# Kernel optimization log

Hardware: AMD Instinct MI355X
Metric: run time of the kernel (lower is better)

## Reference

```python
import jax, jax.numpy as jnp
import numpy as np

EMBED_DIM = 1024
HEAD_DIM = 64
B, T = 4, 4096


def setup_inputs() -> dict:
    key = jax.random.key(0)
    kx, kq, kk, kv = jax.random.split(key, 4)
    x = jax.random.normal(kx, (B, T, EMBED_DIM), dtype=jnp.float32)
    # nn.Linear weights, stored transposed as (in, out) for x @ W
    s = 1.0 / np.sqrt(EMBED_DIM)
    Wq = jax.random.normal(kq, (EMBED_DIM, HEAD_DIM), dtype=jnp.float32) * s
    Wk = jax.random.normal(kk, (EMBED_DIM, HEAD_DIM), dtype=jnp.float32) * s
    Wv = jax.random.normal(kv, (EMBED_DIM, HEAD_DIM), dtype=jnp.float32) * s
    return {"x": x, "Wq": Wq, "Wk": Wk, "Wv": Wv}


def reference(x, Wq, Wk, Wv):
    Bc, Tc, C = x.shape
    Q = x @ Wq  # [B, T, H]
    K = x @ Wk
    V = x @ Wv
    # NOTE: original scales by embedding_dim C, not head_dim
    scores = jnp.einsum('bqh,bkh->bqk', Q, K) / jnp.sqrt(jnp.float32(C))
    causal = jnp.tril(jnp.ones((Tc, Tc), dtype=bool))
    scores = jnp.where(causal, scores, -jnp.inf)
    attn = jax.nn.softmax(scores, axis=-1)
    return jnp.einsum('bqk,bkh->bqh', attn, V)
```

## Files before the change

kernel.cpp:

```cpp
#include <hip/hip_runtime.h>
#include <hip/hip_bf16.h>
#include <math.h>

typedef __attribute__((ext_vector_type(8))) short bf16x8;
typedef __attribute__((ext_vector_type(4))) float f32x4;

#define MFMA16 __builtin_amdgcn_mfma_f32_16x16x32_bf16

static constexpr int TSEQ = 4096;
static constexpr int EMB = 1024;
static constexpr int HD = 64;

__device__ __forceinline__ unsigned short f2bf(float f) {
    unsigned u = __builtin_bit_cast(unsigned, f);
    u += 0x7fffu + ((u >> 16) & 1u);
    return (unsigned short)(u >> 16);
}
__device__ __forceinline__ int pk2bf(float a, float b) {
    return (int)((unsigned)f2bf(a) | ((unsigned)f2bf(b) << 16));
}

union frag_u { int i[4]; bf16x8 v; };

__global__ void prep_w(const float* __restrict__ Wq, const float* __restrict__ Wk,
                       const float* __restrict__ Wv, unsigned short* __restrict__ Wp) {
    int id = blockIdx.x * 256 + threadIdx.x;
    int wsel = id >> 16;
    int t = id & 65535;
    int k = t >> 6, n0 = t & 63;
    const float* W = (wsel == 0) ? Wq : (wsel == 1) ? Wk : Wv;
    float v = W[t];
    if (wsel == 0) v *= 0.03125f;
    int n = wsel * 64 + n0;
    Wp[(k >> 5) * 6144 + n * 32 + (k & 31)] = f2bf(v);
}

__global__ __launch_bounds__(256, 2) void proj_kernel(const float* __restrict__ X,
        const unsigned short* __restrict__ Wp, unsigned short* __restrict__ Qp,
        unsigned short* __restrict__ Kp, unsigned short* __restrict__ Vp) {
    const int lane = threadIdx.x & 63, wave = threadIdx.x >> 6;
    const int col = lane & 15, quad = lane >> 4;
    const int row0 = blockIdx.x * 32;

    f32x4 acc[2][3];
#pragma unroll
    for (int m = 0; m < 2; m++)
#pragma unroll
        for (int j = 0; j < 3; j++) acc[m][j] = (f32x4)(0.0f);

    const float* xr0 = X + (size_t)(row0 + col) * EMB + quad * 8;
    const float* xr1 = xr0 + 16 * EMB;
    const char* wB = (const char*)Wp + wave * 1024 + col * 64 + quad * 16;

    float4 xa[2][2];
    bf16x8 wf[3];
    xa[0][0] = *(const float4*)(xr0);
    xa[0][1] = *(const float4*)(xr0 + 4);
    xa[1][0] = *(const float4*)(xr1);
    xa[1][1] = *(const float4*)(xr1 + 4);
#pragma unroll
    for (int j = 0; j < 3; j++) wf[j] = *(const bf16x8*)(wB + j * 4096);

#pragma unroll 2
    for (int kc = 0; kc < 32; kc++) {
        float4 xn[2][2];
        bf16x8 wn[3];
        if (kc < 31) {
            const float* p0 = xr0 + (kc + 1) * 32;
            const float* p1 = xr1 + (kc + 1) * 32;
            xn[0][0] = *(const float4*)(p0);
            xn[0][1] = *(const float4*)(p0 + 4);
            xn[1][0] = *(const float4*)(p1);
            xn[1][1] = *(const float4*)(p1 + 4);
            const char* wp = wB + (size_t)(kc + 1) * 12288;
#pragma unroll
            for (int j = 0; j < 3; j++) wn[j] = *(const bf16x8*)(wp + j * 4096);
        }
        frag_u A[2];
#pragma unroll
        for (int m = 0; m < 2; m++) {
            A[m].i[0] = pk2bf(xa[m][0].x, xa[m][0].y);
            A[m].i[1] = pk2bf(xa[m][0].z, xa[m][0].w);
            A[m].i[2] = pk2bf(xa[m][1].x, xa[m][1].y);
            A[m].i[3] = pk2bf(xa[m][1].z, xa[m][1].w);
        }
#pragma unroll
        for (int m = 0; m < 2; m++)
#pragma unroll
            for (int j = 0; j < 3; j++)
                acc[m][j] = MFMA16(A[m].v, wf[j], acc[m][j], 0, 0, 0);
        if (kc < 31) {
#pragma unroll
            for (int m = 0; m < 2; m++)
#pragma unroll
                for (int h = 0; h < 2; h++) xa[m][h] = xn[m][h];
#pragma unroll
            for (int j = 0; j < 3; j++) wf[j] = wn[j];
        }
    }

    const int tile0 = blockIdx.x * 2;
    const int c = blockIdx.x;
#pragma unroll
    for (int m = 0; m < 2; m++) {
#pragma unroll
        for (int r = 0; r < 4; r++)
            Qp[(tile0 + m) * 1024 + (wave >> 1) * 512 + (quad * 4 + r) * 32 +
               ((wave & 1) * 2 + (col >> 3)) * 8 + (col & 7)] = f2bf(acc[m][0][r]);
#pragma unroll
        for (int r = 0; r < 4; r++)
            Kp[((c * 2 + m) * 2 + (wave >> 1)) * 512 + (quad * 4 + r) * 32 +
               ((wave & 1) * 2 + (col >> 3)) * 8 + (col & 7)] = f2bf(acc[m][1][r]);
        ushort4 pk;
        pk.x = f2bf(acc[m][2][0]); pk.y = f2bf(acc[m][2][1]);
        pk.z = f2bf(acc[m][2][2]); pk.w = f2bf(acc[m][2][3]);
        *(ushort4*)&Vp[c * 2048 + wave * 512 + col * 32 + m * 16 + quad * 4] = pk;
    }
}

__global__ __launch_bounds__(512, 4) void attn_kernel(const unsigned short* __restrict__ Qp,
        const unsigned short* __restrict__ Kp, const unsigned short* __restrict__ Vp,
        float* __restrict__ Out) {
    __shared__ float cmb[4][2][64][20];
    __shared__ unsigned short plds[8][2][640];
    const int lane = threadIdx.x & 63, wave = threadIdx.x >> 6;
    const int col = lane & 15, quad = lane >> 4;
    const int batch = blockIdx.x & 3;
    const int ti = 127 - (blockIdx.x >> 2);
    const int q0 = ti * 32;
    const size_t bT = (size_t)batch * TSEQ;
    const int fragoff = col * 64 + quad * 16;

    const char* QpB = (const char*)Qp;
    const char* KpB = (const char*)Kp;
    const char* VpB = (const char*)Vp;
    const int gt = (int)((bT + q0) >> 4);
    const int c0 = (int)(bT >> 5);

    bf16x8 aq[2][2];
#pragma unroll
    for (int m = 0; m < 2; m++)
#pragma unroll
        for (int h = 0; h < 2; h++)
            aq[m][h] = *(const bf16x8*)(QpB + (size_t)((gt + m) * 2 + h) * 1024 + fragoff);

    f32x4 o[2][4];
    f32x4 lsum[2];
#pragma unroll
    for (int m = 0; m < 2; m++) {
        lsum[m] = (f32x4)(0.0f);
#pragma unroll
        for (int t = 0; t < 4; t++) o[m][t] = (f32x4)(0.0f);
    }

    for (int c = wave; c <= ti; c += 8) {
        const char* kb = KpB + (size_t)(c0 + c) * 4096;
        const char* vb = VpB + (size_t)(c0 + c) * 4096;
        bf16x8 bk[2][2], bv[4];
#pragma unroll
        for (int j = 0; j < 2; j++)
#pragma unroll
            for (int h = 0; h < 2; h++)
                bk[j][h] = *(const bf16x8*)(kb + j * 2048 + h * 1024 + fragoff);
#pragma unroll
        for (int t = 0; t < 4; t++)
            bv[t] = *(const bf16x8*)(vb + t * 1024 + fragoff);

        f32x4 s[2][2];
#pragma unroll
        for (int m = 0; m < 2; m++)
#pragma unroll
            for (int j = 0; j < 2; j++) {
                f32x4 a = MFMA16(aq[m][0], bk[j][0], (f32x4)(0.0f), 0, 0, 0);
                s[m][j] = MFMA16(aq[m][1], bk[j][1], a, 0, 0, 0);
            }
        const bool diag = (c == ti);
#pragma unroll
        for (int m = 0; m < 2; m++)
#pragma unroll
            for (int j = 0; j < 2; j++)
#pragma unroll
                for (int r = 0; r < 4; r++) {
                    float v = s[m][j][r];
                    if (diag && (j * 16 + col > m * 16 + quad * 4 + r)) v = -INFINITY;
                    const float p = __expf(v);
                    lsum[m][r] += p;
                    plds[wave][m][(quad * 4 + r) * 40 + j * 16 + col] =
                        (unsigned short)(__builtin_bit_cast(unsigned, p) >> 16);
                }
        bf16x8 pa[2];
#pragma unroll
        for (int m = 0; m < 2; m++)
            pa[m] = *(const bf16x8*)(&plds[wave][m][col * 40 + quad * 8]);
#pragma unroll
        for (int m = 0; m < 2; m++)
#pragma unroll
            for (int t = 0; t < 4; t++)
                o[m][t] = MFMA16(pa[m], bv[t], o[m][t], 0, 0, 0);
    }

    auto wr = [&](int s) {
#pragma unroll
        for (int m = 0; m < 2; m++) {
#pragma unroll
            for (int t = 0; t < 4; t++)
                *(f32x4*)&cmb[s][m][lane][t * 4] = o[m][t];
            *(f32x4*)&cmb[s][m][lane][16] = lsum[m];
        }
    };
    auto rd = [&](int s) {
#pragma unroll
        for (int m = 0; m < 2; m++) {
#pragma unroll
            for (int t = 0; t < 4; t++)
                o[m][t] += *(const f32x4*)&cmb[s][m][lane][t * 4];
            lsum[m] += *(const f32x4*)&cmb[s][m][lane][16];
        }
    };
    if (wave >= 4) wr(wave - 4);
    __syncthreads();
    if (wave < 4) rd(wave);
    __syncthreads();
    if (wave == 2 || wave == 3) wr(wave);
    __syncthreads();
    if (wave < 2) rd(wave + 2);
    __syncthreads();
    if (wave == 1) wr(1);
    __syncthreads();
    if (wave == 0) {
        rd(1);
#pragma unroll
        for (int off = 1; off < 16; off <<= 1)
#pragma unroll
            for (int m = 0; m < 2; m++)
#pragma unroll
                for (int r = 0; r < 4; r++)
                    lsum[m][r] += __shfl_xor(lsum[m][r], off, 64);
#pragma unroll
        for (int m = 0; m < 2; m++)
#pragma unroll
            for (int r = 0; r < 4; r++) {
                const float inv = 1.0f / lsum[m][r];
                const size_t orow = (bT + q0 + m * 16 + quad * 4 + r) * HD;
#pragma unroll
                for (int t = 0; t < 4; t++)
                    Out[orow + t * 16 + col] = o[m][t][r] * inv;
            }
    }
}

extern "C" void kernel_launch(void* const* d_in, const int* in_sizes, int n_in,
                              void* d_out, int out_size, void* d_ws, size_t ws_size,
                              hipStream_t stream) {
    const float* x  = (const float*)d_in[0];
    const float* Wq = (const float*)d_in[1];
    const float* Wk = (const float*)d_in[2];
    const float* Wv = (const float*)d_in[3];
    float* out = (float*)d_out;

    char* w = (char*)d_ws;
    unsigned short* Wp = (unsigned short*)(w);
    unsigned short* Qp = (unsigned short*)(w + (512 << 10));
    unsigned short* Kp = (unsigned short*)(w + (512 << 10) + (2 << 20));
    unsigned short* Vp = (unsigned short*)(w + (512 << 10) + (4 << 20));

    hipLaunchKernelGGL(prep_w, dim3(768), dim3(256), 0, stream, Wq, Wk, Wv, Wp);
    hipLaunchKernelGGL(proj_kernel, dim3(512), dim3(256), 0, stream, x, Wp, Qp, Kp, Vp);
    hipLaunchKernelGGL(attn_kernel, dim3(512), dim3(512), 0, stream, Qp, Kp, Vp, out);
}
```

Measured before the change: 162.7 us.

## Stage projection weights in LDS via async global_load_lds with split-K waves

The projection kernel now doubles its block to 512 threads and splits the K dimension between two wave groups. Each stage of packed weights is copied straight into double-buffered shared memory with global_load_lds, and the two partial accumulators are summed through LDS before the store. prep_w writes the weights in a fragment-friendly layout so each lane reads one contiguous 16-byte fragment. The goal is to cut redundant global weight loads and add memory parallelism, at the cost of two barriers per stage and an extra LDS reduction.

```diff
diff --git a/kernel.cpp b/kernel.cpp
--- a/kernel.cpp
+++ b/kernel.cpp
@@ -21,6 +21,12 @@
 }
 
 union frag_u { int i[4]; bf16x8 v; };
+
+__device__ __forceinline__ void gll16(const void* g, void* l) {
+    __builtin_amdgcn_global_load_lds(
+        (const __attribute__((address_space(1))) void*)g,
+        (__attribute__((address_space(3))) void*)l, 16, 0, 0);
+}
 
 __global__ void prep_w(const float* __restrict__ Wq, const float* __restrict__ Wk,
                        const float* __restrict__ Wv, unsigned short* __restrict__ Wp) {
@@ -32,14 +38,18 @@
     float v = W[t];
     if (wsel == 0) v *= 0.03125f;
     int n = wsel * 64 + n0;
-    Wp[(k >> 5) * 6144 + n * 32 + (k & 31)] = f2bf(v);
-}
-
-__global__ __launch_bounds__(256, 2) void proj_kernel(const float* __restrict__ X,
+    Wp[(k >> 5) * 6144 + (n >> 4) * 512 + ((k >> 3) & 3) * 128 + (n & 15) * 8 + (k & 7)] = f2bf(v);
+}
+
+__global__ __launch_bounds__(512, 4) void proj_kernel(const float* __restrict__ X,
         const unsigned short* __restrict__ Wp, unsigned short* __restrict__ Qp,
         unsigned short* __restrict__ Kp, unsigned short* __restrict__ Vp) {
-    const int lane = threadIdx.x & 63, wave = threadIdx.x >> 6;
+    __shared__ unsigned short wlds[2][12288];
+
+    const int tid = threadIdx.x;
+    const int lane = tid & 63, wave = tid >> 6;
     const int col = lane & 15, quad = lane >> 4;
+    const int par = wave >> 2, ng = wave & 3;
     const int row0 = blockIdx.x * 32;
 
     f32x4 acc[2][3];
@@ -48,73 +58,97 @@
 #pragma unroll
         for (int j = 0; j < 3; j++) acc[m][j] = (f32x4)(0.0f);
 
-    const float* xr0 = X + (size_t)(row0 + col) * EMB + quad * 8;
-    const float* xr1 = xr0 + 16 * EMB;
-    const char* wB = (const char*)Wp + wave * 1024 + col * 64 + quad * 16;
-
-    float4 xa[2][2];
-    bf16x8 wf[3];
-    xa[0][0] = *(const float4*)(xr0);
-    xa[0][1] = *(const float4*)(xr0 + 4);
-    xa[1][0] = *(const float4*)(xr1);
-    xa[1][1] = *(const float4*)(xr1 + 4);
-#pragma unroll
-    for (int j = 0; j < 3; j++) wf[j] = *(const bf16x8*)(wB + j * 4096);
-
-#pragma unroll 2
-    for (int kc = 0; kc < 32; kc++) {
-        float4 xn[2][2];
-        bf16x8 wn[3];
-        if (kc < 31) {
-            const float* p0 = xr0 + (kc + 1) * 32;
-            const float* p1 = xr1 + (kc + 1) * 32;
-            xn[0][0] = *(const float4*)(p0);
-            xn[0][1] = *(const float4*)(p0 + 4);
-            xn[1][0] = *(const float4*)(p1);
-            xn[1][1] = *(const float4*)(p1 + 4);
-            const char* wp = wB + (size_t)(kc + 1) * 12288;
-#pragma unroll
-            for (int j = 0; j < 3; j++) wn[j] = *(const bf16x8*)(wp + j * 4096);
-        }
-        frag_u A[2];
+    const char* wsrc = (const char*)Wp + lane * 16;
+    auto stageW = [&](int s, int b) {
+        const char* src = wsrc + (size_t)(2 * s + par) * 12288;
+        char* d = (char*)&wlds[b][0] + par * 12288;
+        gll16(src + ng * 1024,       d + ng * 1024);
+        gll16(src + (4 + ng) * 1024, d + (4 + ng) * 1024);
+        gll16(src + (8 + ng) * 1024, d + (8 + ng) * 1024);
+    };
+
+    const float* xs0 = X + (size_t)(row0 + col) * EMB + par * 32 + quad * 8;
+    const float* xs1 = xs0 + 16 * EMB;
+
+    auto compute = [&](int b, float4 a00, float4 a01, float4 a10, float4 a11) {
+        frag_u A0, A1;
+        A0.i[0] = pk2bf(a00.x, a00.y); A0.i[1] = pk2bf(a00.z, a00.w);
+        A0.i[2] = pk2bf(a01.x, a01.y); A0.i[3] = pk2bf(a01.z, a01.w);
+        A1.i[0] = pk2bf(a10.x, a10.y); A1.i[1] = pk2bf(a10.z, a10.w);
+        A1.i[2] = pk2bf(a11.x, a11.y); A1.i[3] = pk2bf(a11.z, a11.w);
+        const char* wb = (const char*)&wlds[b][0] + par * 12288 + lane * 16;
+        const bf16x8 W0 = *(const bf16x8*)(wb + ng * 1024);
+        const bf16x8 W1 = *(const bf16x8*)(wb + (4 + ng) * 1024);
+        const bf16x8 W2 = *(const bf16x8*)(wb + (8 + ng) * 1024);
+        acc[0][0] = MFMA16(A0.v, W0, acc[0][0], 0, 0, 0);
+        acc[0][1] = MFMA16(A0.v, W1, acc[0][1], 0, 0, 0);
+        acc[0][2] = MFMA16(A0.v, W2, acc[0][2], 0, 0, 0);
+        acc[1][0] = MFMA16(A1.v, W0, acc[1][0], 0, 0, 0);
+        acc[1][1] = MFMA16(A1.v, W1, acc[1][1], 0, 0, 0);
+        acc[1][2] = MFMA16(A1.v, W2, acc[1][2], 0, 0, 0);
+    };
+
+    float4 p00, p01, p10, p11, q00, q01, q10, q11;
+    stageW(0, 0);
+    p00 = *(const float4*)(xs0);
+    p01 = *(const float4*)(xs0 + 4);
+    p10 = *(const float4*)(xs1);
+    p11 = *(const float4*)(xs1 + 4);
+    __syncthreads();
+
+    for (int si = 0; si < 8; si++) {
+        const int s0 = si * 2;
+        if (s0 + 1 < 16) {
+            q00 = *(const float4*)(xs0 + (s0 + 1) * 64);
+            q01 = *(const float4*)(xs0 + (s0 + 1) * 64 + 4);
+            q10 = *(const float4*)(xs1 + (s0 + 1) * 64);
+            q11 = *(const float4*)(xs1 + (s0 + 1) * 64 + 4);
+            stageW(s0 + 1, 1);
+        }
+        compute(0, p00, p01, p10, p11);
+        __syncthreads();
+        if (s0 + 2 < 16) {
+            p00 = *(const float4*)(xs0 + (s0 + 2) * 64);
+            p01 = *(const float4*)(xs0 + (s0 + 2) * 64 + 4);
+            p10 = *(const float4*)(xs1 + (s0 + 2) * 64);
+            p11 = *(const float4*)(xs1 + (s0 + 2) * 64 + 4);
+            stageW(s0 + 2, 0);
+        }
+        compute(1, q00, q01, q10, q11);
+        __syncthreads();
+    }
+
+    f32x4* ex = (f32x4*)&wlds[0][0];
+    if (par == 1) {
+#pragma unroll
+        for (int m = 0; m < 2; m++)
+#pragma unroll
+            for (int j = 0; j < 3; j++)
+                ex[(m * 3 + j) * 256 + ng * 64 + lane] = acc[m][j];
+    }
+    __syncthreads();
+    if (par == 0) {
+#pragma unroll
+        for (int m = 0; m < 2; m++)
+#pragma unroll
+            for (int j = 0; j < 3; j++)
+                acc[m][j] += ex[(m * 3 + j) * 256 + ng * 64 + lane];
 #pragma unroll
         for (int m = 0; m < 2; m++) {
-            A[m].i[0] = pk2bf(xa[m][0].x, xa[m][0].y);
-            A[m].i[1] = pk2bf(xa[m][0].z, xa[m][0].w);
-            A[m].i[2] = pk2bf(xa[m][1].x, xa[m][1].y);
-            A[m].i[3] = pk2bf(xa[m][1].z, xa[m][1].w);
-        }
-#pragma unroll
-        for (int m = 0; m < 2; m++)
-#pragma unroll
-            for (int j = 0; j < 3; j++)
-                acc[m][j] = MFMA16(A[m].v, wf[j], acc[m][j], 0, 0, 0);
-        if (kc < 31) {
-#pragma unroll
-            for (int m = 0; m < 2; m++)
-#pragma unroll
-                for (int h = 0; h < 2; h++) xa[m][h] = xn[m][h];
-#pragma unroll
-            for (int j = 0; j < 3; j++) wf[j] = wn[j];
-        }
-    }
-
-    const int tile0 = blockIdx.x * 2;
-    const int c = blockIdx.x;
-#pragma unroll
-    for (int m = 0; m < 2; m++) {
-#pragma unroll
-        for (int r = 0; r < 4; r++)
-            Qp[(tile0 + m) * 1024 + (wave >> 1) * 512 + (quad * 4 + r) * 32 +
-               ((wave & 1) * 2 + (col >> 3)) * 8 + (col & 7)] = f2bf(acc[m][0][r]);
-#pragma unroll
-        for (int r = 0; r < 4; r++)
-            Kp[((c * 2 + m) * 2 + (wave >> 1)) * 512 + (quad * 4 + r) * 32 +
-               ((wave & 1) * 2 + (col >> 3)) * 8 + (col & 7)] = f2bf(acc[m][1][r]);
-        ushort4 pk;
-        pk.x = f2bf(acc[m][2][0]); pk.y = f2bf(acc[m][2][1]);
-        pk.z = f2bf(acc[m][2][2]); pk.w = f2bf(acc[m][2][3]);
-        *(ushort4*)&Vp[c * 2048 + wave * 512 + col * 32 + m * 16 + quad * 4] = pk;
+            const int tile = blockIdx.x * 2 + m;
+#pragma unroll
+            for (int r = 0; r < 4; r++)
+                Qp[tile * 1024 + (ng >> 1) * 512 + (quad * 4 + r) * 32 +
+                   ((ng & 1) * 2 + (col >> 3)) * 8 + (col & 7)] = f2bf(acc[m][0][r]);
+#pragma unroll
+            for (int r = 0; r < 4; r++)
+                Kp[(tile * 2 + (ng >> 1)) * 512 + (quad * 4 + r) * 32 +
+                   ((ng & 1) * 2 + (col >> 3)) * 8 + (col & 7)] = f2bf(acc[m][1][r]);
+            ushort4 pk;
+            pk.x = f2bf(acc[m][2][0]); pk.y = f2bf(acc[m][2][1]);
+            pk.z = f2bf(acc[m][2][2]); pk.w = f2bf(acc[m][2][3]);
+            *(ushort4*)&Vp[blockIdx.x * 2048 + ng * 512 + col * 32 + m * 16 + quad * 4] = pk;
+        }
     }
 }
 
@@ -265,6 +299,6 @@
     unsigned short* Vp = (unsigned short*)(w + (512 << 10) + (4 << 20));
 
     hipLaunchKernelGGL(prep_w, dim3(768), dim3(256), 0, stream, Wq, Wk, Wv, Wp);
-    hipLaunchKernelGGL(proj_kernel, dim3(512), dim3(256), 0, stream, x, Wp, Qp, Kp, Vp);
+    hipLaunchKernelGGL(proj_kernel, dim3(512), dim3(512), 0, stream, x, Wp, Qp, Kp, Vp);
     hipLaunchKernelGGL(attn_kernel, dim3(512), dim3(512), 0, stream, Qp, Kp, Vp, out);
 }
```

Measured after the change: 153.9 us. 1.06x faster.
